# Kernel tuning notes

Measured on AMD Instinct MI355X. Metric: run time of the kernel, lower is better.

The kernel has to match this reference:

```python
import jax, jax.numpy as jnp
import numpy as np

EPS = 1e-7
MIN_NORM = 1e-15
PROJ_EPS = 1e-5
NEG_SLOPE = 0.2
HEADS = 4


def artanh(x):
    return jnp.arctanh(jnp.clip(x, -1.0 + EPS, 1.0 - EPS))


def _norm(x):
    return jnp.clip(jnp.linalg.norm(x, axis=-1, keepdims=True), MIN_NORM)


def proj(x):
    # project onto Poincare ball (c=1)
    n = _norm(x)
    maxn = 1.0 - PROJ_EPS
    return jnp.where(n > maxn, x / n * maxn, x)


def expmap0(u):
    n = _norm(u)
    return jnp.tanh(n) * u / n


def logmap0(x):
    n = _norm(x)
    return artanh(n) * x / n


def mobius_add(x, y):
    x2 = jnp.sum(x * x, axis=-1, keepdims=True)
    y2 = jnp.sum(y * y, axis=-1, keepdims=True)
    xy = jnp.sum(x * y, axis=-1, keepdims=True)
    num = (1.0 + 2.0 * xy + y2) * x + (1.0 - x2) * y
    den = 1.0 + 2.0 * xy + x2 * y2
    return num / jnp.clip(den, MIN_NORM)


def pdist(x, y):
    # Poincare distance, c=1 -> [...,] scalar
    ma = mobius_add(-x, y)
    return 2.0 * artanh(jnp.linalg.norm(ma, axis=-1))


def mobius_scalar_mul(r, x):
    n = _norm(x)
    return jnp.tanh(r * artanh(n)) * x / n


def mobius_matvec(W, x):
    # x: [N,din], W: [dout,din]
    mx = x @ W.T
    n_x = _norm(x)
    n_mx = _norm(mx)
    return jnp.tanh(n_mx / n_x * artanh(n_x)) * mx / n_mx


def segment_softmax(logits, seg, num_segments):
    m = jax.ops.segment_max(logits, seg, num_segments=num_segments)
    m = jnp.where(jnp.isfinite(m), m, 0.0)
    e = jnp.exp(logits - m[seg])
    s = jax.ops.segment_sum(e, seg, num_segments=num_segments)
    return e / (s[seg] + 1e-16)


def setup_inputs() -> dict:
    N, E, D = 50000, 500000, 128
    H = HEADS
    Dh = D // H
    ks = jax.random.split(jax.random.key(0), 12)
    # edges without self-loops (reference re-adds them, mirroring remove/add_self_loops)
    src = jax.random.randint(ks[0], (E,), 0, N)
    off = jax.random.randint(ks[1], (E,), 1, N)
    dst = (src + off) % N
    edge_index = jnp.stack([src, dst]).astype(jnp.int32)
    x_e = 0.1 * jax.random.normal(ks[2], (N, D), dtype=jnp.float32)
    x_h = proj(expmap0(0.05 * jax.random.normal(ks[3], (N, D), dtype=jnp.float32)))
    sc = 1.0 / np.sqrt(D)
    W_e = sc * jax.random.normal(ks[4], (D, D), dtype=jnp.float32)
    b_lin_e = jnp.zeros((D,), jnp.float32)
    att_e = 0.1 * jax.random.normal(ks[5], (1, H, 2 * Dh), dtype=jnp.float32)
    b_e = jnp.zeros((D,), jnp.float32)
    W_h = sc * jax.random.normal(ks[6], (D, D), dtype=jnp.float32)
    b_lin_h = jnp.zeros((D,), jnp.float32)
    att_h = 0.1 * jax.random.normal(ks[7], (1, H, 2 * Dh), dtype=jnp.float32)
    b_h = jnp.zeros((D,), jnp.float32)
    att_hf = 0.1 * jax.random.normal(ks[8], (1, 1), dtype=jnp.float32)
    att_ef = 0.1 * jax.random.normal(ks[9], (1, 1), dtype=jnp.float32)
    return {"x_e": x_e, "x_h": x_h, "edge_index": edge_index,
            "W_e": W_e, "b_lin_e": b_lin_e, "att_e": att_e, "b_e": b_e,
            "W_h": W_h, "b_lin_h": b_lin_h, "att_h": att_h, "b_h": b_h,
            "att_hf": att_hf, "att_ef": att_ef}


def reference(x_e, x_h, edge_index, W_e, b_lin_e, att_e, b_e,
              W_h, b_lin_h, att_h, b_h, att_hf, att_ef):
    N, D = x_e.shape
    H = HEADS
    Dh = att_e.shape[-1] // 2
    loop = jnp.arange(N, dtype=edge_index.dtype)
    src = jnp.concatenate([edge_index[0], loop])  # j (source)
    dst = jnp.concatenate([edge_index[1], loop])  # i (target, softmax segment)

    # ---- Euclidean GAT branch (GATConv) ----
    xe = (x_e @ W_e.T + b_lin_e).reshape(N, H, Dh)
    a_i = jnp.sum(xe * att_e[:, :, :Dh], axis=-1)  # [N,H] target part
    a_j = jnp.sum(xe * att_e[:, :, Dh:], axis=-1)  # [N,H] source part
    alpha = jax.nn.leaky_relu(a_i[dst] + a_j[src], NEG_SLOPE)  # [E',H]
    alpha = segment_softmax(alpha, dst, N)
    agg = jax.ops.segment_sum(xe[src] * alpha[:, :, None], dst, num_segments=N)
    e_out = jax.nn.relu(agg.reshape(N, H * Dh) + b_e)

    # ---- Hyperbolic GAT branch (HGATConv with HypLinear) ----
    mv = proj(mobius_matvec(W_h, x_h))
    hb = proj(expmap0(b_lin_h))  # proj_tan0 is identity on Poincare ball
    xh = proj(mobius_add(mv, hb))  # [N,D] hyperbolic points (original_x)
    lx = logmap0(xh).reshape(N, H, Dh)
    hi = jnp.sum(lx * att_h[:, :, :Dh], axis=-1)
    hj = jnp.sum(lx * att_h[:, :, Dh:], axis=-1)
    alpha_h = hi[dst] + hj[src]  # [E',H]
    d = pdist(xh[dst], xh[src])  # [E'] hyperbolic edge distances
    d = segment_softmax(d, dst, N)[:, None]
    alpha_h = jax.nn.leaky_relu(alpha_h * d, NEG_SLOPE)
    alpha_h = segment_softmax(alpha_h, dst, N)
    agg_h = jax.ops.segment_sum(lx[src] * alpha_h[:, :, None], dst, num_segments=N)
    out_t = jax.nn.relu(agg_h.reshape(N, H * Dh) + b_h)  # tangent at origin
    h_out = proj(expmap0(out_t))

    # ---- HFusion: fuse Euclidean into hyperbolic ----
    ye = proj(expmap0(e_out))
    dist_f = (pdist(h_out, ye) * att_hf[0, 0])[:, None]  # [N,1]
    xe2 = proj(mobius_scalar_mul(dist_f, ye))
    h_fused = proj(mobius_add(h_out, xe2))

    # ---- EFusion: fuse hyperbolic into Euclidean ----
    lh = logmap0(h_out)
    de = (jnp.sum((lh - e_out) ** 2, axis=-1) * att_ef[0, 0])[:, None]
    e_fused = e_out + de * lh

    return jnp.stack([h_fused, e_fused])  # [2,N,D]
```

## Files before the change

kernel.cpp:

```cpp
#include <hip/hip_runtime.h>
#include <hip/hip_fp16.h>
#include <math.h>

typedef _Float16 h2 __attribute__((ext_vector_type(2)));
typedef _Float16 h8 __attribute__((ext_vector_type(8)));
typedef float f32x4 __attribute__((ext_vector_type(4)));

#define MAXN_BALL (1.0f - 1e-5f)
#define ART_CLIP  (1.0f - 1e-7f)
#define MAXD 48

__device__ __forceinline__ float f_rcp(float x)  { return __builtin_amdgcn_rcpf(x); }
__device__ __forceinline__ float f_exp(float x)  { return __expf(x); }
__device__ __forceinline__ float f_log(float x)  { return __logf(x); }
__device__ __forceinline__ float f_tanh(float x) {
    float ax = fabsf(x);
    float e = __expf(2.f * ax);
    float t = 1.f - 2.f * f_rcp(e + 1.f);
    return copysignf(t, x);
}
__device__ __forceinline__ float f_atanh(float x) {
    x = fminf(x, ART_CLIP);
    return 0.5f * f_log((1.f + x) * f_rcp(1.f - x));
}
__device__ __forceinline__ float leaky(float x) { return x > 0.0f ? x : 0.2f * x; }

union F4H8 { float4 f; h2 h[4]; };
union F2H4 { float2 f; h2 h[2]; };
union H8U  { h8 v; h2 h[4]; };
union H8F  { float4 f; h8 v; h2 h[4]; };

__device__ __forceinline__ h2 pk16(float x, float y) {
    union { decltype(__builtin_amdgcn_cvt_pkrtz(0.f, 0.f)) a; h2 b; } u;
    u.a = __builtin_amdgcn_cvt_pkrtz(x, y);
    return u.b;
}

__global__ __launch_bounds__(256) void k_wcvt(const float* __restrict__ W0,
                                              const float* __restrict__ W1,
                                              h2* __restrict__ W16,
                                              int* __restrict__ counts,
                                              int N, int cblocks) {
    int b = blockIdx.x, t = threadIdx.x;
    if (b < cblocks) {
        int zi = b * 256 + t;
        if (zi < N) counts[zi] = 0;
        return;
    }
    int tw = (b - cblocks) * 256 + t;
    const float* W = (tw < 2048) ? W0 : W1;
    int c = (tw & 2047) * 8;
    float4 a = *(const float4*)(W + c);
    float4 bb = *(const float4*)(W + c + 4);
    F4H8 u;
    u.h[0] = pk16(a.x, a.y);  u.h[1] = pk16(a.z, a.w);
    u.h[2] = pk16(bb.x, bb.y); u.h[3] = pk16(bb.z, bb.w);
    *(float4*)&W16[(tw >> 11) * 8192 + (c >> 1)] = u.f;
}

__global__ __launch_bounds__(256) void k_prep_fused(
        const float* __restrict__ x_e, const float* __restrict__ x_h,
        const h2* __restrict__ W16,
        const float* __restrict__ b_lin_e, const float* __restrict__ b_lin_h,
        const float* __restrict__ att_e, const float* __restrict__ att_h,
        h2* __restrict__ xe16, h2* __restrict__ xh16,
        float* __restrict__ aux_j, float* __restrict__ aux_i,
        const int* __restrict__ ei, int* __restrict__ counts,
        int* __restrict__ srcs, int N, int E) {
    int t = threadIdx.x;
    if (blockIdx.y == 1) {
        int idx = blockIdx.x * 256 + t;
        if (idx < E + N) {
            int s, d;
            if (idx < E) { s = ei[idx]; d = ei[E + idx]; } else { s = d = idx - E; }
            int p = atomicAdd(&counts[d], 1);
            if (p < MAXD) srcs[d * MAXD + p] = s;
        }
        return;
    }
    int wv = t >> 6, l = t & 63;
    int rt = blockIdx.x * 4 + wv;
    if (rt * 16 >= N) return;
    int lane16 = l & 15, quad = l >> 4;
    int r = rt * 16 + lane16;
    int rr = (r < N) ? r : (N - 1);

    const float* Xrow = &x_e[(size_t)rr * 128 + quad * 8];
    H8U bfr[4];
#pragma unroll
    for (int ks = 0; ks < 4; ++ks) {
        float4 xa = *(const float4*)(Xrow + ks * 32);
        float4 xb = *(const float4*)(Xrow + ks * 32 + 4);
        bfr[ks].h[0] = pk16(xa.x, xa.y); bfr[ks].h[1] = pk16(xa.z, xa.w);
        bfr[ks].h[2] = pk16(xb.x, xb.y); bfr[ks].h[3] = pk16(xb.z, xb.w);
    }
    float pi[4] = {0.f, 0.f, 0.f, 0.f}, pj[4] = {0.f, 0.f, 0.f, 0.f};
#pragma unroll
    for (int ct = 0; ct < 8; ++ct) {
        const h2* Wrow = &W16[(ct * 16 + lane16) * 64 + quad * 4];
        f32x4 acc = {0.f, 0.f, 0.f, 0.f};
#pragma unroll
        for (int ks = 0; ks < 4; ++ks) {
            H8F a;
            a.f = *(const float4*)(Wrow + ks * 16);
            acc = __builtin_amdgcn_mfma_f32_16x16x32_f16(a.v, bfr[ks].v, acc, 0, 0, 0);
        }
        int obase = ct * 16 + quad * 4;
        float4 bb = *(const float4*)&b_lin_e[obase];
        F2H4 u;
        u.h[0] = pk16(acc[0] + bb.x, acc[1] + bb.y);
        u.h[1] = pk16(acc[2] + bb.z, acc[3] + bb.w);
        if (r < N) *(float2*)&xe16[(size_t)r * 64 + (obase >> 1)] = u.f;
        float4 xe4 = make_float4((float)u.h[0].x, (float)u.h[0].y,
                                 (float)u.h[1].x, (float)u.h[1].y);
        int hd = ct >> 1, w0 = (ct & 1) * 16 + quad * 4;
        float4 aT = *(const float4*)&att_e[hd * 64 + w0];
        float4 aS = *(const float4*)&att_e[hd * 64 + 32 + w0];
        pi[hd] += xe4.x * aT.x + xe4.y * aT.y + xe4.z * aT.z + xe4.w * aT.w;
        pj[hd] += xe4.x * aS.x + xe4.y * aS.y + xe4.z * aS.z + xe4.w * aS.w;
    }

    const float* Xrow1 = &x_h[(size_t)rr * 128 + quad * 8];
    float nx2 = 0.f;
#pragma unroll
    for (int ks = 0; ks < 4; ++ks) {
        float4 xa = *(const float4*)(Xrow1 + ks * 32);
        float4 xb = *(const float4*)(Xrow1 + ks * 32 + 4);
        nx2 += xa.x * xa.x + xa.y * xa.y + xa.z * xa.z + xa.w * xa.w
             + xb.x * xb.x + xb.y * xb.y + xb.z * xb.z + xb.w * xb.w;
        bfr[ks].h[0] = pk16(xa.x, xa.y); bfr[ks].h[1] = pk16(xa.z, xa.w);
        bfr[ks].h[2] = pk16(xb.x, xb.y); bfr[ks].h[3] = pk16(xb.z, xb.w);
    }
    f32x4 mx[8];
    float4 bh[8];
    float nmx2 = 0.f, dmb = 0.f, nb2 = 0.f;
#pragma unroll
    for (int ct = 0; ct < 8; ++ct) {
        const h2* Wrow = &W16[8192 + (ct * 16 + lane16) * 64 + quad * 4];
        f32x4 acc = {0.f, 0.f, 0.f, 0.f};
#pragma unroll
        for (int ks = 0; ks < 4; ++ks) {
            H8F a;
            a.f = *(const float4*)(Wrow + ks * 16);
            acc = __builtin_amdgcn_mfma_f32_16x16x32_f16(a.v, bfr[ks].v, acc, 0, 0, 0);
        }
        mx[ct] = acc;
        int obase = ct * 16 + quad * 4;
        float4 bv = *(const float4*)&b_lin_h[obase];
        bh[ct] = bv;
        nmx2 += acc[0] * acc[0] + acc[1] * acc[1] + acc[2] * acc[2] + acc[3] * acc[3];
        dmb  += acc[0] * bv.x + acc[1] * bv.y + acc[2] * bv.z + acc[3] * bv.w;
        nb2  += bv.x * bv.x + bv.y * bv.y + bv.z * bv.z + bv.w * bv.w;
    }
#pragma unroll
    for (int m = 16; m <= 32; m <<= 1) {
        nx2 += __shfl_xor(nx2, m, 64); nmx2 += __shfl_xor(nmx2, m, 64);
        dmb += __shfl_xor(dmb, m, 64); nb2  += __shfl_xor(nb2, m, 64);
    }

    float nxr = sqrtf(nx2),  nxc = fmaxf(nxr, 1e-15f);
    float nmxr = sqrtf(nmx2), nmxc = fmaxf(nmxr, 1e-15f);
    float tt = f_tanh(nmxc * f_rcp(nxc) * f_atanh(nxc));
    float c_m = tt * f_rcp(nmxc);
    float nmv = tt * (nmxr * f_rcp(nmxc));
    if (nmv > MAXN_BALL) { c_m *= MAXN_BALL / nmv; nmv = MAXN_BALL; }

    float nbr = sqrtf(nb2), nbc = fmaxf(nbr, 1e-15f);
    float tb = f_tanh(nbc);
    float c_b = tb * f_rcp(nbc);
    float nhb = tb * (nbr * f_rcp(nbc));
    if (nhb > MAXN_BALL) { c_b *= MAXN_BALL / nhb; nhb = MAXN_BALL; }

    float xy = c_m * c_b * dmb;
    float x2 = nmv * nmv, y2 = nhb * nhb;
    float den = fmaxf(1.f + 2.f * xy + x2 * y2, 1e-15f);
    float rden = f_rcp(den);
    float al = (1.f + 2.f * xy + y2) * c_m * rden;
    float be = (1.f - x2) * c_b * rden;
    float nr2 = al * al * nmx2 + 2.f * al * be * dmb + be * be * nb2;
    float nrr = sqrtf(nr2);
    if (nrr > MAXN_BALL) { float sc = MAXN_BALL / nrr; al *= sc; be *= sc; }

    float nr2r = 0.f;
    float sT[4] = {0.f, 0.f, 0.f, 0.f}, sS[4] = {0.f, 0.f, 0.f, 0.f};
#pragma unroll
    for (int ct = 0; ct < 8; ++ct) {
        float4 resv;
        resv.x = al * mx[ct][0] + be * bh[ct].x;
        resv.y = al * mx[ct][1] + be * bh[ct].y;
        resv.z = al * mx[ct][2] + be * bh[ct].z;
        resv.w = al * mx[ct][3] + be * bh[ct].w;
        F2H4 u;
        u.h[0] = pk16(resv.x, resv.y);
        u.h[1] = pk16(resv.z, resv.w);
        int obase = ct * 16 + quad * 4;
        if (r < N) *(float2*)&xh16[(size_t)r * 64 + (obase >> 1)] = u.f;
        float4 rv = make_float4((float)u.h[0].x, (float)u.h[0].y,
                                (float)u.h[1].x, (float)u.h[1].y);
        nr2r += rv.x * rv.x + rv.y * rv.y + rv.z * rv.z + rv.w * rv.w;
        int hd = ct >> 1, w0 = (ct & 1) * 16 + quad * 4;
        float4 hT = *(const float4*)&att_h[hd * 64 + w0];
        float4 hS = *(const float4*)&att_h[hd * 64 + 32 + w0];
        sT[hd] += rv.x * hT.x + rv.y * hT.y + rv.z * hT.z + rv.w * hT.w;
        sS[hd] += rv.x * hS.x + rv.y * hS.y + rv.z * hS.z + rv.w * hS.w;
    }
#pragma unroll
    for (int m = 16; m <= 32; m <<= 1) {
        nr2r += __shfl_xor(nr2r, m, 64);
#pragma unroll
        for (int hd = 0; hd < 4; ++hd) {
            pi[hd] += __shfl_xor(pi[hd], m, 64);
            pj[hd] += __shfl_xor(pj[hd], m, 64);
            sT[hd] += __shfl_xor(sT[hd], m, 64);
            sS[hd] += __shfl_xor(sS[hd], m, 64);
        }
    }
    float nrrr = sqrtf(nr2r);
    float nnc = fmaxf(nrrr, 1e-15f);
    float lam = f_atanh(nnc) * f_rcp(nnc);

    if (quad == 0 && r < N) {
        float4 qj4 = make_float4(lam * sS[0], lam * sS[1], lam * sS[2], lam * sS[3]);
        float4 pj4 = make_float4(pj[0], pj[1], pj[2], pj[3]);
        *(float4*)&aux_j[(size_t)r * 16]     = qj4;
        *(float4*)&aux_j[(size_t)r * 16 + 4] = pj4;
        *(float2*)&aux_j[(size_t)r * 16 + 8] = make_float2(lam, nr2r);
        float4 qi4 = make_float4(lam * sT[0], lam * sT[1], lam * sT[2], lam * sT[3]);
        float4 pi4 = make_float4(pi[0], pi[1], pi[2], pi[3]);
        *(float4*)&aux_i[(size_t)r * 8]     = qi4;
        *(float4*)&aux_i[(size_t)r * 8 + 4] = pi4;
    }
}

__global__ __launch_bounds__(256) void k_node_final(
    const h2* __restrict__ xh16, const float* __restrict__ aux_j,
    const float* __restrict__ aux_i, const h2* __restrict__ xe16,
    const int* __restrict__ counts, const int* __restrict__ srcs,
    const float* __restrict__ b_e, const float* __restrict__ b_h,
    const float* __restrict__ att_hf, const float* __restrict__ att_ef,
    float* __restrict__ out, int N) {
    __shared__ int   s_src_all[8][MAXD];
    __shared__ float s_d_all[8][MAXD];
    __shared__ float s_ah_all[8][MAXD * 4];
    __shared__ float s_ae_all[8][MAXD * 4];

    int t = threadIdx.x;
    int sl = t & 31, ni = t >> 5;
    int i = blockIdx.x * 8 + ni;
    if (i >= N) return;
    int*   s_src = s_src_all[ni];
    float* s_d   = s_d_all[ni];
    float* s_ah  = s_ah_all[ni];
    float* s_ae  = s_ae_all[ni];

    int deg = counts[i];
    if (deg > MAXD) deg = MAXD;
    if (sl < deg)      s_src[sl]      = srcs[i * MAXD + sl];
    if (sl + 32 < deg) s_src[sl + 32] = srcs[i * MAXD + sl + 32];

    float x2i = aux_j[(uint32_t)i * 16u + 9u];
    {
        int g = sl & 7, sub = sl >> 3;
        uint32_t goff = (uint32_t)(g * 8);
        const h2* xi = &xh16[(uint32_t)i * 64u + goff];
        F4H8 us0, us1;
        us0.f = *(const float4*)xi;
        us1.f = *(const float4*)(xi + 4);
        for (int p = 0; p * 4 < deg; ++p) {
            int e = p * 4 + sub;
            bool act = e < deg;
            float dot = 0.f;
            int j = 0;
            if (act) {
                j = s_src[e];
                uint32_t oj = (uint32_t)j * 64u + goff;
                F4H8 ua, ub;
                ua.f = *(const float4*)&xh16[oj];
                ub.f = *(const float4*)&xh16[oj + 4u];
#pragma unroll
                for (int k = 0; k < 4; ++k) dot = __builtin_amdgcn_fdot2(ua.h[k], us0.h[k], dot, false);
#pragma unroll
                for (int k = 0; k < 4; ++k) dot = __builtin_amdgcn_fdot2(ub.h[k], us1.h[k], dot, false);
            }
            dot += __shfl_xor(dot, 1, 64);
            dot += __shfl_xor(dot, 2, 64);
            dot += __shfl_xor(dot, 4, 64);
            if (act && g == 0) {
                float y2 = aux_j[(uint32_t)j * 16u + 9u];
                float xy = dot;
                float A = 1.f - 2.f * xy + y2;
                float B = 1.f - x2i;
                float den = fmaxf(1.f - 2.f * xy + x2i * y2, 1e-15f);
                float num2 = fmaxf(A * A * x2i - 2.f * A * B * xy + B * B * y2, 0.f);
                float nma = fminf(sqrtf(num2) * f_rcp(den), ART_CLIP);
                s_d[e] = f_log((1.f + nma) * f_rcp(1.f - nma));
            }
        }
    }

    float eA = (sl < deg)      ? f_exp(s_d[sl])      : 0.f;
    float eB = (sl + 32 < deg) ? f_exp(s_d[sl + 32]) : 0.f;
    float ssum = eA + eB;
#pragma unroll
    for (int m = 16; m >= 1; m >>= 1) ssum += __shfl_xor(ssum, m, 64);
    float dinv = f_rcp(ssum + 1e-16f);

    float4 hi4 = *(const float4*)&aux_i[(uint32_t)i * 8u];
    float4 ai4 = *(const float4*)&aux_i[(uint32_t)i * 8u + 4u];
    float4 vh_s[2], ve_s[2];
    float lam_s[2] = {0.f, 0.f};
    float4 sh = make_float4(0.f, 0.f, 0.f, 0.f), se = sh;
#pragma unroll
    for (int s = 0; s < 2; ++s) {
        int e = sl + 32 * s;
        if (e < deg) {
            int j = s_src[e];
            float ds = (s ? eB : eA) * dinv;
            uint32_t oj = (uint32_t)j * 16u;
            float4 hj4 = *(const float4*)&aux_j[oj];
            float4 aj4 = *(const float4*)&aux_j[oj + 4u];
            lam_s[s] = aux_j[oj + 8u];
            float4 vh, ve;
            vh.x = f_exp(leaky((hi4.x + hj4.x) * ds));
            vh.y = f_exp(leaky((hi4.y + hj4.y) * ds));
            vh.z = f_exp(leaky((hi4.z + hj4.z) * ds));
            vh.w = f_exp(leaky((hi4.w + hj4.w) * ds));
            ve.x = f_exp(leaky(ai4.x + aj4.x));
            ve.y = f_exp(leaky(ai4.y + aj4.y));
            ve.z = f_exp(leaky(ai4.z + aj4.z));
            ve.w = f_exp(leaky(ai4.w + aj4.w));
            vh_s[s] = vh; ve_s[s] = ve;
            sh.x += vh.x; sh.y += vh.y; sh.z += vh.z; sh.w += vh.w;
            se.x += ve.x; se.y += ve.y; se.z += ve.z; se.w += ve.w;
        }
    }
#pragma unroll
    for (int m = 16; m >= 1; m >>= 1) {
        sh.x += __shfl_xor(sh.x, m, 64); sh.y += __shfl_xor(sh.y, m, 64);
        sh.z += __shfl_xor(sh.z, m, 64); sh.w += __shfl_xor(sh.w, m, 64);
        se.x += __shfl_xor(se.x, m, 64); se.y += __shfl_xor(se.y, m, 64);
        se.z += __shfl_xor(se.z, m, 64); se.w += __shfl_xor(se.w, m, 64);
    }
    float4 rh = make_float4(f_rcp(sh.x + 1e-16f), f_rcp(sh.y + 1e-16f),
                            f_rcp(sh.z + 1e-16f), f_rcp(sh.w + 1e-16f));
    float4 re = make_float4(f_rcp(se.x + 1e-16f), f_rcp(se.y + 1e-16f),
                            f_rcp(se.z + 1e-16f), f_rcp(se.w + 1e-16f));
#pragma unroll
    for (int s = 0; s < 2; ++s) {
        int e = sl + 32 * s;
        if (e < deg) {
            float lamj = lam_s[s];
            float4 vh = vh_s[s], ve = ve_s[s];
            vh.x *= rh.x * lamj; vh.y *= rh.y * lamj; vh.z *= rh.z * lamj; vh.w *= rh.w * lamj;
            ve.x *= re.x; ve.y *= re.y; ve.z *= re.z; ve.w *= re.w;
            *(float4*)&s_ah[e * 4] = vh;
            *(float4*)&s_ae[e * 4] = ve;
        }
    }

    int hq = sl >> 3;
    uint32_t dsl = 2u * (uint32_t)sl;
    float4 aE = make_float4(0.f, 0.f, 0.f, 0.f), aH = aE;
    int e = 0;
    for (; e + 3 < deg; e += 4) {
        int j0 = s_src[e], j1 = s_src[e + 1], j2 = s_src[e + 2], j3 = s_src[e + 3];
        uint32_t o0 = (uint32_t)j0 * 64u + dsl, o1 = (uint32_t)j1 * 64u + dsl;
        uint32_t o2 = (uint32_t)j2 * 64u + dsl, o3 = (uint32_t)j3 * 64u + dsl;
        F2H4 ux0, uh0, ux1, uh1, ux2, uh2, ux3, uh3;
        ux0.f = *(const float2*)&xe16[o0]; uh0.f = *(const float2*)&xh16[o0];
        ux1.f = *(const float2*)&xe16[o1]; uh1.f = *(const float2*)&xh16[o1];
        ux2.f = *(const float2*)&xe16[o2]; uh2.f = *(const float2*)&xh16[o2];
        ux3.f = *(const float2*)&xe16[o3]; uh3.f = *(const float2*)&xh16[o3];
        float we0 = s_ae[e * 4 + hq],       wh0 = s_ah[e * 4 + hq];
        float we1 = s_ae[(e + 1) * 4 + hq], wh1 = s_ah[(e + 1) * 4 + hq];
        float we2 = s_ae[(e + 2) * 4 + hq], wh2 = s_ah[(e + 2) * 4 + hq];
        float we3 = s_ae[(e + 3) * 4 + hq], wh3 = s_ah[(e + 3) * 4 + hq];
        aE.x += we0 * (float)ux0.h[0].x + we1 * (float)ux1.h[0].x;
        aE.y += we0 * (float)ux0.h[0].y + we1 * (float)ux1.h[0].y;
        aE.z += we0 * (float)ux0.h[1].x + we1 * (float)ux1.h[1].x;
        aE.w += we0 * (float)ux0.h[1].y + we1 * (float)ux1.h[1].y;
        aH.x += wh0 * (float)uh0.h[0].x + wh1 * (float)uh1.h[0].x;
        aH.y += wh0 * (float)uh0.h[0].y + wh1 * (float)uh1.h[0].y;
        aH.z += wh0 * (float)uh0.h[1].x + wh1 * (float)uh1.h[1].x;
        aH.w += wh0 * (float)uh0.h[1].y + wh1 * (float)uh1.h[1].y;
        aE.x += we2 * (float)ux2.h[0].x + we3 * (float)ux3.h[0].x;
        aE.y += we2 * (float)ux2.h[0].y + we3 * (float)ux3.h[0].y;
        aE.z += we2 * (float)ux2.h[1].x + we3 * (float)ux3.h[1].x;
        aE.w += we2 * (float)ux2.h[1].y + we3 * (float)ux3.h[1].y;
        aH.x += wh2 * (float)uh2.h[0].x + wh3 * (float)uh3.h[0].x;
        aH.y += wh2 * (float)uh2.h[0].y + wh3 * (float)uh3.h[0].y;
        aH.z += wh2 * (float)uh2.h[1].x + wh3 * (float)uh3.h[1].x;
        aH.w += wh2 * (float)uh2.h[1].y + wh3 * (float)uh3.h[1].y;
    }
    for (; e + 1 < deg; e += 2) {
        int j0 = s_src[e], j1 = s_src[e + 1];
        uint32_t o0 = (uint32_t)j0 * 64u + dsl, o1 = (uint32_t)j1 * 64u + dsl;
        F2H4 ux0, uh0, ux1, uh1;
        ux0.f = *(const float2*)&xe16[o0]; uh0.f = *(const float2*)&xh16[o0];
        ux1.f = *(const float2*)&xe16[o1]; uh1.f = *(const float2*)&xh16[o1];
        float we0 = s_ae[e * 4 + hq], wh0 = s_ah[e * 4 + hq];
        float we1 = s_ae[(e + 1) * 4 + hq], wh1 = s_ah[(e + 1) * 4 + hq];
        aE.x += we0 * (float)ux0.h[0].x + we1 * (float)ux1.h[0].x;
        aE.y += we0 * (float)ux0.h[0].y + we1 * (float)ux1.h[0].y;
        aE.z += we0 * (float)ux0.h[1].x + we1 * (float)ux1.h[1].x;
        aE.w += we0 * (float)ux0.h[1].y + we1 * (float)ux1.h[1].y;
        aH.x += wh0 * (float)uh0.h[0].x + wh1 * (float)uh1.h[0].x;
        aH.y += wh0 * (float)uh0.h[0].y + wh1 * (float)uh1.h[0].y;
        aH.z += wh0 * (float)uh0.h[1].x + wh1 * (float)uh1.h[1].x;
        aH.w += wh0 * (float)uh0.h[1].y + wh1 * (float)uh1.h[1].y;
    }
    if (e < deg) {
        int j = s_src[e];
        uint32_t oj = (uint32_t)j * 64u + dsl;
        F2H4 ux, uh;
        ux.f = *(const float2*)&xe16[oj];
        uh.f = *(const float2*)&xh16[oj];
        float we = s_ae[e * 4 + hq], wh = s_ah[e * 4 + hq];
        aE.x += we * (float)ux.h[0].x; aE.y += we * (float)ux.h[0].y;
        aE.z += we * (float)ux.h[1].x; aE.w += we * (float)ux.h[1].y;
        aH.x += wh * (float)uh.h[0].x; aH.y += wh * (float)uh.h[0].y;
        aH.z += wh * (float)uh.h[1].x; aH.w += wh * (float)uh.h[1].y;
    }

    float4 be4 = *(const float4*)&b_e[4 * sl];
    float4 bh4 = *(const float4*)&b_h[4 * sl];
    float4 eo, ot;
    eo.x = fmaxf(aE.x + be4.x, 0.f); eo.y = fmaxf(aE.y + be4.y, 0.f);
    eo.z = fmaxf(aE.z + be4.z, 0.f); eo.w = fmaxf(aE.w + be4.w, 0.f);
    ot.x = fmaxf(aH.x + bh4.x, 0.f); ot.y = fmaxf(aH.y + bh4.y, 0.f);
    ot.z = fmaxf(aH.z + bh4.z, 0.f); ot.w = fmaxf(aH.w + bh4.w, 0.f);
    float n2  = ot.x * ot.x + ot.y * ot.y + ot.z * ot.z + ot.w * ot.w;
    float ne2 = eo.x * eo.x + eo.y * eo.y + eo.z * eo.z + eo.w * eo.w;
    float dot3 = ot.x * eo.x + ot.y * eo.y + ot.z * eo.z + ot.w * eo.w;
#pragma unroll
    for (int m = 16; m >= 1; m >>= 1) {
        n2 += __shfl_xor(n2, m, 64); ne2 += __shfl_xor(ne2, m, 64); dot3 += __shfl_xor(dot3, m, 64);
    }

    float n_raw = sqrtf(n2), n_c = fmaxf(n_raw, 1e-15f);
    float th = f_tanh(n_c);
    float c_h = th * f_rcp(n_c);
    float nh = th * (n_raw * f_rcp(n_c));
    if (nh > MAXN_BALL) { c_h *= MAXN_BALL / nh; nh = MAXN_BALL; }

    float nE_raw = sqrtf(ne2), nE_c = fmaxf(nE_raw, 1e-15f);
    float tE = f_tanh(nE_c);
    float c_e = tE * f_rcp(nE_c);
    float ny = tE * (nE_raw * f_rcp(nE_c));
    if (ny > MAXN_BALL) { c_e *= MAXN_BALL / ny; ny = MAXN_BALL; }

    float xyv = c_h * c_e * dot3;
    float x2f = nh * nh, y2f = ny * ny;
    float A = 1.f - 2.f * xyv + y2f, B = 1.f - x2f;
    float den = fmaxf(1.f - 2.f * xyv + x2f * y2f, 1e-15f);
    float num2 = fmaxf(A * A * x2f - 2.f * A * B * xyv + B * B * y2f, 0.f);
    float nma = fminf(sqrtf(num2) * f_rcp(den), ART_CLIP);
    float distf = f_log((1.f + nma) * f_rcp(1.f - nma)) * att_hf[0];
    float nyc = fmaxf(ny, 1e-15f);
    float s1 = f_tanh(distf * f_atanh(nyc)) * f_rcp(nyc);
    float nxe2 = fabsf(s1) * ny;
    if (nxe2 > MAXN_BALL) { s1 *= MAXN_BALL / nxe2; nxe2 = MAXN_BALL; }
    float xy2 = s1 * xyv;
    float y22 = nxe2 * nxe2;
    float rden2 = f_rcp(fmaxf(1.f + 2.f * xy2 + x2f * y22, 1e-15f));
    float alpha = (1.f + 2.f * xy2 + y22) * rden2 * c_h;
    float beta  = (1.f - x2f) * s1 * rden2 * c_e;
    float nf2 = alpha * alpha * n2 + 2.f * alpha * beta * dot3 + beta * beta * ne2;
    float nf = sqrtf(nf2);
    if (nf > MAXN_BALL) { float sc = MAXN_BALL / nf; alpha *= sc; beta *= sc; }

    float nhc = fmaxf(nh, 1e-15f);
    float gam = f_atanh(nhc) * f_rcp(nhc) * c_h;
    float de2 = gam * gam * n2 - 2.f * gam * dot3 + ne2;
    float dg = de2 * att_ef[0] * gam;

    float4 o1;
    o1.x = alpha * ot.x + beta * eo.x; o1.y = alpha * ot.y + beta * eo.y;
    o1.z = alpha * ot.z + beta * eo.z; o1.w = alpha * ot.w + beta * eo.w;
    *(float4*)&out[(size_t)i * 128 + 4 * sl] = o1;
    float4 o2;
    o2.x = eo.x + dg * ot.x; o2.y = eo.y + dg * ot.y;
    o2.z = eo.z + dg * ot.z; o2.w = eo.w + dg * ot.w;
    *(float4*)&out[(size_t)N * 128 + (size_t)i * 128 + 4 * sl] = o2;
}

extern "C" void kernel_launch(void* const* d_in, const int* in_sizes, int n_in,
                              void* d_out, int out_size, void* d_ws, size_t ws_size,
                              hipStream_t stream) {
    const float* x_e      = (const float*)d_in[0];
    const float* x_h      = (const float*)d_in[1];
    const int*   ei       = (const int*)d_in[2];
    const float* W_e      = (const float*)d_in[3];
    const float* b_lin_e  = (const float*)d_in[4];
    const float* att_e    = (const float*)d_in[5];
    const float* b_e      = (const float*)d_in[6];
    const float* W_h      = (const float*)d_in[7];
    const float* b_lin_h  = (const float*)d_in[8];
    const float* att_h    = (const float*)d_in[9];
    const float* b_h      = (const float*)d_in[10];
    const float* att_hf   = (const float*)d_in[11];
    const float* att_ef   = (const float*)d_in[12];

    int N = in_sizes[0] / 128;
    int E = in_sizes[2] / 2;
    int EN = E + N;

    char* ws = (char*)d_ws;
    size_t off = 0;
    auto alloc = [&](size_t bytes) -> void* {
        void* p = ws + off;
        off = (off + bytes + 255) & ~(size_t)255;
        return p;
    };
    h2*    W16   = (h2*)alloc((size_t)2 * 8192 * 4);
    h2*    xe16  = (h2*)alloc((size_t)N * 128 * 2);
    h2*    xh16  = (h2*)alloc((size_t)N * 128 * 2);
    float* aux_j = (float*)alloc((size_t)N * 16 * 4);
    float* aux_i = (float*)alloc((size_t)N * 8 * 4);
    int*   counts= (int*)alloc((size_t)N * 4);
    int*   srcs  = (int*)alloc((size_t)N * MAXD * 4);

    int cblocks = (N + 255) / 256;
    k_wcvt<<<cblocks + 16, 256, 0, stream>>>(W_e, W_h, W16, counts, N, cblocks);

    int rtiles = (N + 15) / 16;
    int rblocks = (rtiles + 3) / 4;
    int eblocks = (EN + 255) / 256;
    int gx = rblocks > eblocks ? rblocks : eblocks;
    dim3 pgrid(gx, 2);
    k_prep_fused<<<pgrid, 256, 0, stream>>>(x_e, x_h, W16, b_lin_e, b_lin_h,
                                            att_e, att_h, xe16, xh16, aux_j, aux_i,
                                            ei, counts, srcs, N, E);

    int fblocks = (N + 7) / 8;
    k_node_final<<<fblocks, 256, 0, stream>>>(xh16, aux_j, aux_i, xe16,
                                              counts, srcs, b_e, b_h, att_hf, att_ef,
                                              (float*)d_out, N);
}
```

Baseline: 252.7 us.

## Interleave fp16 Euclidean and hyperbolic node features into one array

Stores the projected Euclidean and hyperbolic fp16 features interleaved per 4-column chunk in a single row-major buffer, so each gather in the aggregation loop fetches both with one 16-byte load instead of two 8-byte loads from separate arrays. The prep kernel keeps the Euclidean results in registers until the hyperbolic ones are ready and writes them together. The distance dot-product gathers now read strided 8-byte pieces instead of contiguous 16-byte pieces, which may cost some efficiency there.

Result: slower. 263.0 us (+4.1%).

```diff
diff --git a/kernel.cpp b/kernel.cpp
--- a/kernel.cpp
+++ b/kernel.cpp
@@ -63,7 +63,7 @@
         const h2* __restrict__ W16,
         const float* __restrict__ b_lin_e, const float* __restrict__ b_lin_h,
         const float* __restrict__ att_e, const float* __restrict__ att_h,
-        h2* __restrict__ xe16, h2* __restrict__ xh16,
+        h2* __restrict__ xeh,
         float* __restrict__ aux_j, float* __restrict__ aux_i,
         const int* __restrict__ ei, int* __restrict__ counts,
         int* __restrict__ srcs, int N, int E) {
@@ -95,6 +95,7 @@
         bfr[ks].h[2] = pk16(xb.x, xb.y); bfr[ks].h[3] = pk16(xb.z, xb.w);
     }
     float pi[4] = {0.f, 0.f, 0.f, 0.f}, pj[4] = {0.f, 0.f, 0.f, 0.f};
+    F2H4 xeH[8];
 #pragma unroll
     for (int ct = 0; ct < 8; ++ct) {
         const h2* Wrow = &W16[(ct * 16 + lane16) * 64 + quad * 4];
@@ -107,12 +108,10 @@
         }
         int obase = ct * 16 + quad * 4;
         float4 bb = *(const float4*)&b_lin_e[obase];
-        F2H4 u;
-        u.h[0] = pk16(acc[0] + bb.x, acc[1] + bb.y);
-        u.h[1] = pk16(acc[2] + bb.z, acc[3] + bb.w);
-        if (r < N) *(float2*)&xe16[(size_t)r * 64 + (obase >> 1)] = u.f;
-        float4 xe4 = make_float4((float)u.h[0].x, (float)u.h[0].y,
-                                 (float)u.h[1].x, (float)u.h[1].y);
+        xeH[ct].h[0] = pk16(acc[0] + bb.x, acc[1] + bb.y);
+        xeH[ct].h[1] = pk16(acc[2] + bb.z, acc[3] + bb.w);
+        float4 xe4 = make_float4((float)xeH[ct].h[0].x, (float)xeH[ct].h[0].y,
+                                 (float)xeH[ct].h[1].x, (float)xeH[ct].h[1].y);
         int hd = ct >> 1, w0 = (ct & 1) * 16 + quad * 4;
         float4 aT = *(const float4*)&att_e[hd * 64 + w0];
         float4 aS = *(const float4*)&att_e[hd * 64 + 32 + w0];
@@ -190,13 +189,14 @@
         resv.y = al * mx[ct][1] + be * bh[ct].y;
         resv.z = al * mx[ct][2] + be * bh[ct].z;
         resv.w = al * mx[ct][3] + be * bh[ct].w;
-        F2H4 u;
-        u.h[0] = pk16(resv.x, resv.y);
-        u.h[1] = pk16(resv.z, resv.w);
-        int obase = ct * 16 + quad * 4;
-        if (r < N) *(float2*)&xh16[(size_t)r * 64 + (obase >> 1)] = u.f;
-        float4 rv = make_float4((float)u.h[0].x, (float)u.h[0].y,
-                                (float)u.h[1].x, (float)u.h[1].y);
+        F4H8 w;
+        w.h[0] = xeH[ct].h[0];
+        w.h[1] = xeH[ct].h[1];
+        w.h[2] = pk16(resv.x, resv.y);
+        w.h[3] = pk16(resv.z, resv.w);
+        if (r < N) *(float4*)&xeh[(size_t)r * 128 + 16 * ct + 4 * quad] = w.f;
+        float4 rv = make_float4((float)w.h[2].x, (float)w.h[2].y,
+                                (float)w.h[3].x, (float)w.h[3].y);
         nr2r += rv.x * rv.x + rv.y * rv.y + rv.z * rv.z + rv.w * rv.w;
         int hd = ct >> 1, w0 = (ct & 1) * 16 + quad * 4;
         float4 hT = *(const float4*)&att_h[hd * 64 + w0];
@@ -233,8 +233,8 @@
 }
 
 __global__ __launch_bounds__(256) void k_node_final(
-    const h2* __restrict__ xh16, const float* __restrict__ aux_j,
-    const float* __restrict__ aux_i, const h2* __restrict__ xe16,
+    const h2* __restrict__ xeh, const float* __restrict__ aux_j,
+    const float* __restrict__ aux_i,
     const int* __restrict__ counts, const int* __restrict__ srcs,
     const float* __restrict__ b_e, const float* __restrict__ b_h,
     const float* __restrict__ att_hf, const float* __restrict__ att_ef,
@@ -261,11 +261,13 @@
     float x2i = aux_j[(uint32_t)i * 16u + 9u];
     {
         int g = sl & 7, sub = sl >> 3;
-        uint32_t goff = (uint32_t)(g * 8);
-        const h2* xi = &xh16[(uint32_t)i * 64u + goff];
-        F4H8 us0, us1;
-        us0.f = *(const float4*)xi;
-        us1.f = *(const float4*)(xi + 4);
+        uint32_t gbase = (uint32_t)g * 16u + 2u;
+        const h2* xi = &xeh[(uint32_t)i * 128u + gbase];
+        F2H4 us[4];
+        us[0].f = *(const float2*)(xi);
+        us[1].f = *(const float2*)(xi + 4);
+        us[2].f = *(const float2*)(xi + 8);
+        us[3].f = *(const float2*)(xi + 12);
         for (int p = 0; p * 4 < deg; ++p) {
             int e = p * 4 + sub;
             bool act = e < deg;
@@ -273,14 +275,20 @@
             int j = 0;
             if (act) {
                 j = s_src[e];
-                uint32_t oj = (uint32_t)j * 64u + goff;
-                F4H8 ua, ub;
-                ua.f = *(const float4*)&xh16[oj];
-                ub.f = *(const float4*)&xh16[oj + 4u];
-#pragma unroll
-                for (int k = 0; k < 4; ++k) dot = __builtin_amdgcn_fdot2(ua.h[k], us0.h[k], dot, false);
-#pragma unroll
-                for (int k = 0; k < 4; ++k) dot = __builtin_amdgcn_fdot2(ub.h[k], us1.h[k], dot, false);
+                const h2* xp = &xeh[(uint32_t)j * 128u + gbase];
+                F2H4 ua0, ua1, ua2, ua3;
+                ua0.f = *(const float2*)(xp);
+                ua1.f = *(const float2*)(xp + 4);
+                ua2.f = *(const float2*)(xp + 8);
+                ua3.f = *(const float2*)(xp + 12);
+                dot = __builtin_amdgcn_fdot2(ua0.h[0], us[0].h[0], dot, false);
+                dot = __builtin_amdgcn_fdot2(ua0.h[1], us[0].h[1], dot, false);
+                dot = __builtin_amdgcn_fdot2(ua1.h[0], us[1].h[0], dot, false);
+                dot = __builtin_amdgcn_fdot2(ua1.h[1], us[1].h[1], dot, false);
+                dot = __builtin_amdgcn_fdot2(ua2.h[0], us[2].h[0], dot, false);
+                dot = __builtin_amdgcn_fdot2(ua2.h[1], us[2].h[1], dot, false);
+                dot = __builtin_amdgcn_fdot2(ua3.h[0], us[3].h[0], dot, false);
+                dot = __builtin_amdgcn_fdot2(ua3.h[1], us[3].h[1], dot, false);
             }
             dot += __shfl_xor(dot, 1, 64);
             dot += __shfl_xor(dot, 2, 64);
@@ -359,67 +367,62 @@
     }
 
     int hq = sl >> 3;
-    uint32_t dsl = 2u * (uint32_t)sl;
+    uint32_t dsl = 4u * (uint32_t)sl;
     float4 aE = make_float4(0.f, 0.f, 0.f, 0.f), aH = aE;
     int e = 0;
     for (; e + 3 < deg; e += 4) {
         int j0 = s_src[e], j1 = s_src[e + 1], j2 = s_src[e + 2], j3 = s_src[e + 3];
-        uint32_t o0 = (uint32_t)j0 * 64u + dsl, o1 = (uint32_t)j1 * 64u + dsl;
-        uint32_t o2 = (uint32_t)j2 * 64u + dsl, o3 = (uint32_t)j3 * 64u + dsl;
-        F2H4 ux0, uh0, ux1, uh1, ux2, uh2, ux3, uh3;
-        ux0.f = *(const float2*)&xe16[o0]; uh0.f = *(const float2*)&xh16[o0];
-        ux1.f = *(const float2*)&xe16[o1]; uh1.f = *(const float2*)&xh16[o1];
-        ux2.f = *(const float2*)&xe16[o2]; uh2.f = *(const float2*)&xh16[o2];
-        ux3.f = *(const float2*)&xe16[o3]; uh3.f = *(const float2*)&xh16[o3];
+        F4H8 u0, u1, u2, u3;
+        u0.f = *(const float4*)&xeh[(uint32_t)j0 * 128u + dsl];
+        u1.f = *(const float4*)&xeh[(uint32_t)j1 * 128u + dsl];
+        u2.f = *(const float4*)&xeh[(uint32_t)j2 * 128u + dsl];
+        u3.f = *(const float4*)&xeh[(uint32_t)j3 * 128u + dsl];
         float we0 = s_ae[e * 4 + hq],       wh0 = s_ah[e * 4 + hq];
         float we1 = s_ae[(e + 1) * 4 + hq], wh1 = s_ah[(e + 1) * 4 + hq];
         float we2 = s_ae[(e + 2) * 4 + hq], wh2 = s_ah[(e + 2) * 4 + hq];
         float we3 = s_ae[(e + 3) * 4 + hq], wh3 = s_ah[(e + 3) * 4 + hq];
-        aE.x += we0 * (float)ux0.h[0].x + we1 * (float)ux1.h[0].x;
-        aE.y += we0 * (float)ux0.h[0].y + we1 * (float)ux1.h[0].y;
-        aE.z += we0 * (float)ux0.h[1].x + we1 * (float)ux1.h[1].x;
-        aE.w += we0 * (float)ux0.h[1].y + we1 * (float)ux1.h[1].y;
-        aH.x += wh0 * (float)uh0.h[0].x + wh1 * (float)uh1.h[0].x;
-        aH.y += wh0 * (float)uh0.h[0].y + wh1 * (float)uh1.h[0].y;
-        aH.z += wh0 * (float)uh0.h[1].x + wh1 * (float)uh1.h[1].x;
-        aH.w += wh0 * (float)uh0.h[1].y + wh1 * (float)uh1.h[1].y;
-        aE.x += we2 * (float)ux2.h[0].x + we3 * (float)ux3.h[0].x;
-        aE.y += we2 * (float)ux2.h[0].y + we3 * (float)ux3.h[0].y;
-        aE.z += we2 * (float)ux2.h[1].x + we3 * (float)ux3.h[1].x;
-        aE.w += we2 * (float)ux2.h[1].y + we3 * (float)ux3.h[1].y;
-        aH.x += wh2 * (float)uh2.h[0].x + wh3 * (float)uh3.h[0].x;
-        aH.y += wh2 * (float)uh2.h[0].y + wh3 * (float)uh3.h[0].y;
-        aH.z += wh2 * (float)uh2.h[1].x + wh3 * (float)uh3.h[1].x;
-        aH.w += wh2 * (float)uh2.h[1].y + wh3 * (float)uh3.h[1].y;
+        aE.x += we0 * (float)u0.h[0].x + we1 * (float)u1.h[0].x;
+        aE.y += we0 * (float)u0.h[0].y + we1 * (float)u1.h[0].y;
+        aE.z += we0 * (float)u0.h[1].x + we1 * (float)u1.h[1].x;
+        aE.w += we0 * (float)u0.h[1].y + we1 * (float)u1.h[1].y;
+        aH.x += wh0 * (float)u0.h[2].x + wh1 * (float)u1.h[2].x;
+        aH.y += wh0 * (float)u0.h[2].y + wh1 * (float)u1.h[2].y;
+        aH.z += wh0 * (float)u0.h[3].x + wh1 * (float)u1.h[3].x;
+        aH.w += wh0 * (float)u0.h[3].y + wh1 * (float)u1.h[3].y;
+        aE.x += we2 * (float)u2.h[0].x + we3 * (float)u3.h[0].x;
+        aE.y += we2 * (float)u2.h[0].y + we3 * (float)u3.h[0].y;
+        aE.z += we2 * (float)u2.h[1].x + we3 * (float)u3.h[1].x;
+        aE.w += we2 * (float)u2.h[1].y + we3 * (float)u3.h[1].y;
+        aH.x += wh2 * (float)u2.h[2].x + wh3 * (float)u3.h[2].x;
+        aH.y += wh2 * (float)u2.h[2].y + wh3 * (float)u3.h[2].y;
+        aH.z += wh2 * (float)u2.h[3].x + wh3 * (float)u3.h[3].x;
+        aH.w += wh2 * (float)u2.h[3].y + wh3 * (float)u3.h[3].y;
     }
     for (; e + 1 < deg; e += 2) {
         int j0 = s_src[e], j1 = s_src[e + 1];
-        uint32_t o0 = (uint32_t)j0 * 64u + dsl, o1 = (uint32_t)j1 * 64u + dsl;
-        F2H4 ux0, uh0, ux1, uh1;
-        ux0.f = *(const float2*)&xe16[o0]; uh0.f = *(const float2*)&xh16[o0];
-        ux1.f = *(const float2*)&xe16[o1]; uh1.f = *(const float2*)&xh16[o1];
+        F4H8 u0, u1;
+        u0.f = *(const float4*)&xeh[(uint32_t)j0 * 128u + dsl];
+        u1.f = *(const float4*)&xeh[(uint32_t)j1 * 128u + dsl];
         float we0 = s_ae[e * 4 + hq], wh0 = s_ah[e * 4 + hq];
         float we1 = s_ae[(e + 1) * 4 + hq], wh1 = s_ah[(e + 1) * 4 + hq];
-        aE.x += we0 * (float)ux0.h[0].x + we1 * (float)ux1.h[0].x;
-        aE.y += we0 * (float)ux0.h[0].y + we1 * (float)ux1.h[0].y;
-        aE.z += we0 * (float)ux0.h[1].x + we1 * (float)ux1.h[1].x;
-        aE.w += we0 * (float)ux0.h[1].y + we1 * (float)ux1.h[1].y;
-        aH.x += wh0 * (float)uh0.h[0].x + wh1 * (float)uh1.h[0].x;
-        aH.y += wh0 * (float)uh0.h[0].y + wh1 * (float)uh1.h[0].y;
-        aH.z += wh0 * (float)uh0.h[1].x + wh1 * (float)uh1.h[1].x;
-        aH.w += wh0 * (float)uh0.h[1].y + wh1 * (float)uh1.h[1].y;
+        aE.x += we0 * (float)u0.h[0].x + we1 * (float)u1.h[0].x;
+        aE.y += we0 * (float)u0.h[0].y + we1 * (float)u1.h[0].y;
+        aE.z += we0 * (float)u0.h[1].x + we1 * (float)u1.h[1].x;
+        aE.w += we0 * (float)u0.h[1].y + we1 * (float)u1.h[1].y;
+        aH.x += wh0 * (float)u0.h[2].x + wh1 * (float)u1.h[2].x;
+        aH.y += wh0 * (float)u0.h[2].y + wh1 * (float)u1.h[2].y;
+        aH.z += wh0 * (float)u0.h[3].x + wh1 * (float)u1.h[3].x;
+        aH.w += wh0 * (float)u0.h[3].y + wh1 * (float)u1.h[3].y;
     }
     if (e < deg) {
         int j = s_src[e];
-        uint32_t oj = (uint32_t)j * 64u + dsl;
-        F2H4 ux, uh;
-        ux.f = *(const float2*)&xe16[oj];
-        uh.f = *(const float2*)&xh16[oj];
+        F4H8 u0;
+        u0.f = *(const float4*)&xeh[(uint32_t)j * 128u + dsl];
         float we = s_ae[e * 4 + hq], wh = s_ah[e * 4 + hq];
-        aE.x += we * (float)ux.h[0].x; aE.y += we * (float)ux.h[0].y;
-        aE.z += we * (float)ux.h[1].x; aE.w += we * (float)ux.h[1].y;
-        aH.x += wh * (float)uh.h[0].x; aH.y += wh * (float)uh.h[0].y;
-        aH.z += wh * (float)uh.h[1].x; aH.w += wh * (float)uh.h[1].y;
+        aE.x += we * (float)u0.h[0].x; aE.y += we * (float)u0.h[0].y;
+        aE.z += we * (float)u0.h[1].x; aE.w += we * (float)u0.h[1].y;
+        aH.x += wh * (float)u0.h[2].x; aH.y += wh * (float)u0.h[2].y;
+        aH.z += wh * (float)u0.h[3].x; aH.w += wh * (float)u0.h[3].y;
     }
 
     float4 be4 = *(const float4*)&b_e[4 * sl];
@@ -513,8 +516,7 @@
         return p;
     };
     h2*    W16   = (h2*)alloc((size_t)2 * 8192 * 4);
-    h2*    xe16  = (h2*)alloc((size_t)N * 128 * 2);
-    h2*    xh16  = (h2*)alloc((size_t)N * 128 * 2);
+    h2*    xeh   = (h2*)alloc((size_t)N * 128 * 4);
     float* aux_j = (float*)alloc((size_t)N * 16 * 4);
     float* aux_i = (float*)alloc((size_t)N * 8 * 4);
     int*   counts= (int*)alloc((size_t)N * 4);
@@ -529,11 +531,11 @@
     int gx = rblocks > eblocks ? rblocks : eblocks;
     dim3 pgrid(gx, 2);
     k_prep_fused<<<pgrid, 256, 0, stream>>>(x_e, x_h, W16, b_lin_e, b_lin_h,
-                                            att_e, att_h, xe16, xh16, aux_j, aux_i,
+                                            att_e, att_h, xeh, aux_j, aux_i,
                                             ei, counts, srcs, N, E);
 
     int fblocks = (N + 7) / 8;
-    k_node_final<<<fblocks, 256, 0, stream>>>(xh16, aux_j, aux_i, xe16,
+    k_node_final<<<fblocks, 256, 0, stream>>>(xeh, aux_j, aux_i,
                                               counts, srcs, b_e, b_h, att_hf, att_ef,
                                               (float*)d_out, N);
 }
```
